# Performance work log

Measured on AMD Instinct MI355X. Metric: run time of the kernel, lower is better.

## Reference

```python
import jax, jax.numpy as jnp
import numpy as np

PH = 32          # prediction horizon (unroll steps)
HID = 512        # hidden_dim == latent_dim (output fed back as input)
OUT = 2          # output_dim
BS = 2048


def setup_inputs() -> dict:
    key = jax.random.key(0)
    ks = jax.random.split(key, 8)
    s = 1.0 / np.sqrt(HID)
    return {
        "hist": jax.random.normal(ks[0], (BS, 8, 2), dtype=jnp.float32),
        "z": jax.random.normal(ks[1], (BS, 1, HID), dtype=jnp.float32),
        # LSTMCell params (PyTorch layout: [4H, in], gate order i,f,g,o)
        "W_ih": jax.random.uniform(ks[2], (4 * HID, HID), jnp.float32, -s, s),
        "W_hh": jax.random.uniform(ks[3], (4 * HID, HID), jnp.float32, -s, s),
        "b_ih": jax.random.uniform(ks[4], (4 * HID,), jnp.float32, -s, s),
        "b_hh": jax.random.uniform(ks[5], (4 * HID,), jnp.float32, -s, s),
        # dense: hidden_dim -> output_dim
        "W_d": jax.random.uniform(ks[6], (OUT, HID), jnp.float32, -s, s),
        "b_d": jax.random.uniform(ks[7], (OUT,), jnp.float32, -s, s),
    }


def reference(hist, z, W_ih, W_hh, b_ih, b_hh, W_d, b_d):
    bs = z.shape[0]
    x0 = z.reshape(bs, -1)                       # [bs, H]
    h0 = jnp.zeros((bs, HID), dtype=z.dtype)
    c0 = jnp.zeros((bs, HID), dtype=z.dtype)

    def step(carry, _):
        x, h, c = carry
        gates = x @ W_ih.T + b_ih + h @ W_hh.T + b_hh   # [bs, 4H]
        i, f, g, o = jnp.split(gates, 4, axis=-1)
        c_new = jax.nn.sigmoid(f) * c + jax.nn.sigmoid(i) * jnp.tanh(g)
        h_new = jax.nn.sigmoid(o) * jnp.tanh(c_new)
        # output h is fed back as next input
        return (h_new, h_new, c_new), h_new

    _, hs = jax.lax.scan(step, (x0, h0, c0), None, length=PH)  # [PH, bs, H]
    out_all = jnp.swapaxes(hs, 0, 1)                           # [bs, PH, H]
    y = out_all @ W_d.T + b_d                                  # [bs, PH, OUT]
    return y
```

## Files before the change

kernel.cpp:

```cpp
#include <hip/hip_runtime.h>
#include <hip/hip_bf16.h>

#define BS_   2048
#define HID_  512
#define PH_   32

typedef _Float16 half8 __attribute__((ext_vector_type(8)));
typedef float floatx4 __attribute__((ext_vector_type(4)));

__device__ __forceinline__ float sigf(float x) { return 1.f / (1.f + __expf(-x)); }
__device__ __forceinline__ float tanhfast(float x) {
    float e = __expf(2.f * x);
    return 1.f - 2.f / (e + 1.f);
}

__global__ __launch_bounds__(256) void prep_kernel(
    const float* __restrict__ Wih, const float* __restrict__ Whh,
    const float* __restrict__ bih, const float* __restrict__ bhh,
    const float* __restrict__ z,
    _Float16* __restrict__ wih16, _Float16* __restrict__ wsum16,
    _Float16* __restrict__ z16, float* __restrict__ bsum,
    int* __restrict__ cnt)
{
    int i = blockIdx.x * 256 + threadIdx.x;
    if (i < BS_ * HID_) z16[i] = (_Float16)z[i];
    if (i < 4 * HID_ * HID_) {
        float a = Wih[i];
        wih16[i]  = (_Float16)a;
        wsum16[i] = (_Float16)(a + Whh[i]);
    }
    if (i < 4 * HID_) bsum[i] = bih[i] + bhh[i];
    if (i < 256) cnt[i] = 0;
}

__device__ __forceinline__ void stage_weights(_Float16* Wl, const _Float16* Wg,
                                              int j, int tid)
{
#pragma unroll
    for (int rep = 0; rep < 8; ++rep) {
        int idx = rep * 512 + tid;
        int n  = idx >> 6;
        int kb = idx & 63;
        int g  = n >> 4, u = n & 15;
        const half8* src = (const half8*)(Wg + ((size_t)(g * HID_ + j * 16 + u)) * HID_ + kb * 8);
        int phys = (kb & 56) | ((kb & 7) ^ (n & 7));
        *(half8*)((char*)Wl + n * 1024 + phys * 16) = *src;
    }
}

__global__ __launch_bounds__(512, 2) void lstm_persist(
    const _Float16* __restrict__ wih16, const _Float16* __restrict__ wsum16,
    const float* __restrict__ bsum, const _Float16* __restrict__ z16,
    _Float16* __restrict__ hs, int* __restrict__ cnt)
{
    __shared__ _Float16 Wl[64 * 512];

    const int tid  = threadIdx.x;
    const int ib   = blockIdx.x & 7;
    const int j    = blockIdx.x >> 3;
    const int lane = tid & 63;
    const int wv   = tid >> 6;
    const int qw   = lane >> 4;
    const int ln   = lane & 15;
    const int hid  = j * 16 + ln;

    stage_weights(Wl, wih16, j, tid);

    float bias[4];
#pragma unroll
    for (int g = 0; g < 4; ++g) bias[g] = bsum[g * HID_ + hid];

    float c[2][4];
#pragma unroll
    for (int mt = 0; mt < 2; ++mt)
#pragma unroll
        for (int r = 0; r < 4; ++r) c[mt][r] = 0.f;

    const char* Bl = (const char*)Wl;
    const int tE = (qw ^ (ln & 7)) * 16;

    __syncthreads();

    for (int t = 0; t < PH_; ++t) {
        const _Float16* xx = (t == 0) ? z16 : hs + (size_t)(t - 1) * BS_ * HID_;

        if (t >= 1) {
            if (tid == 0) {
                while (__hip_atomic_fetch_add(&cnt[ib * 32 + t - 1], 0,
                                              __ATOMIC_RELAXED,
                                              __HIP_MEMORY_SCOPE_AGENT) < 32) {
                    __builtin_amdgcn_s_sleep(1);
                }
            }
            __syncthreads();
        }

        floatx4 acc[2][4];
#pragma unroll
        for (int mt = 0; mt < 2; ++mt)
#pragma unroll
            for (int g = 0; g < 4; ++g)
                acc[mt][g] = (floatx4){bias[g], bias[g], bias[g], bias[g]};

        const _Float16* A0 = xx + (size_t)(ib * 256 + wv * 32 + ln) * HID_ + qw * 8;

        half8 a0r[4], a1r[4], bA[4], bB[4];
#pragma unroll
        for (int p = 0; p < 4; ++p) {
            a0r[p] = *(const half8*)(A0 + p * 32);
            a1r[p] = *(const half8*)(A0 + 16 * HID_ + p * 32);
        }
#pragma unroll
        for (int g = 0; g < 4; ++g)
            bA[g] = *(const half8*)(Bl + (g * 16 + ln) * 1024 + tE);

#pragma unroll
        for (int kk = 0; kk < 16; ++kk) {
            half8 ca0 = a0r[kk & 3], ca1 = a1r[kk & 3];
            if (kk < 12) {
                a0r[kk & 3] = *(const half8*)(A0 + (kk + 4) * 32);
                a1r[kk & 3] = *(const half8*)(A0 + 16 * HID_ + (kk + 4) * 32);
            }
            half8* cb = (kk & 1) ? bB : bA;
            half8* nb = (kk & 1) ? bA : bB;
            if (kk < 15) {
                int k1 = kk + 1;
#pragma unroll
                for (int g = 0; g < 4; ++g) {
                    int off = (g * 16 + ln) * 1024 + (k1 >> 1) * 128 + (tE ^ ((k1 & 1) << 6));
                    nb[g] = *(const half8*)(Bl + off);
                }
            }
#pragma unroll
            for (int g = 0; g < 4; ++g) {
                acc[0][g] = __builtin_amdgcn_mfma_f32_16x16x32_f16(ca0, cb[g], acc[0][g], 0, 0, 0);
                acc[1][g] = __builtin_amdgcn_mfma_f32_16x16x32_f16(ca1, cb[g], acc[1][g], 0, 0, 0);
            }
        }

        _Float16* hb = hs + (size_t)t * BS_ * HID_
                          + (size_t)(ib * 256 + wv * 32 + qw * 4) * HID_ + hid;
#pragma unroll
        for (int mt = 0; mt < 2; ++mt) {
#pragma unroll
            for (int r = 0; r < 4; ++r) {
                float gi = acc[mt][0][r];
                float gf = acc[mt][1][r];
                float gg = acc[mt][2][r];
                float go = acc[mt][3][r];
                float cn = sigf(gf) * c[mt][r] + sigf(gi) * tanhfast(gg);
                float hn = sigf(go) * tanhfast(cn);
                c[mt][r] = cn;
                _Float16 hf = (_Float16)hn;
                short hv;
                __builtin_memcpy(&hv, &hf, 2);
                __hip_atomic_store((short*)(hb + (size_t)(mt * 16 + r) * HID_), hv,
                                   __ATOMIC_RELAXED, __HIP_MEMORY_SCOPE_AGENT);
            }
        }

        __syncthreads();
        if (t == 0) {
            if (tid == 0)
                __hip_atomic_fetch_add(&cnt[ib * 32], 1,
                                       __ATOMIC_RELAXED, __HIP_MEMORY_SCOPE_AGENT);
            stage_weights(Wl, wsum16, j, tid);
            __syncthreads();
        } else if (t < PH_ - 1) {
            if (tid == 0)
                __hip_atomic_fetch_add(&cnt[ib * 32 + t], 1,
                                       __ATOMIC_RELAXED, __HIP_MEMORY_SCOPE_AGENT);
        }
    }
}

__global__ __launch_bounds__(256) void dense_kernel(
    const _Float16* __restrict__ hs, const float* __restrict__ Wd,
    const float* __restrict__ bd, float* __restrict__ y)
{
    int gw   = (blockIdx.x * 256 + threadIdx.x) >> 6;
    int lane = threadIdx.x & 63;
    int tt = gw & 31, b = gw >> 5;
    half8 h = *(const half8*)(hs + ((size_t)tt * BS_ + b) * HID_ + lane * 8);
    float s0 = 0.f, s1 = 0.f;
#pragma unroll
    for (int k = 0; k < 8; ++k) {
        float hv = (float)h[k];
        s0 += hv * Wd[lane * 8 + k];
        s1 += hv * Wd[HID_ + lane * 8 + k];
    }
#pragma unroll
    for (int m = 32; m >= 1; m >>= 1) {
        s0 += __shfl_xor(s0, m);
        s1 += __shfl_xor(s1, m);
    }
    if (lane == 0) {
        float* o = y + ((size_t)b * PH_ + tt) * 2;
        o[0] = s0 + bd[0];
        o[1] = s1 + bd[1];
    }
}

extern "C" void kernel_launch(void* const* d_in, const int* in_sizes, int n_in,
                              void* d_out, int out_size, void* d_ws, size_t ws_size,
                              hipStream_t stream)
{
    (void)in_sizes; (void)n_in; (void)out_size; (void)ws_size;
    const float* z   = (const float*)d_in[1];
    const float* Wih = (const float*)d_in[2];
    const float* Whh = (const float*)d_in[3];
    const float* bih = (const float*)d_in[4];
    const float* bhh = (const float*)d_in[5];
    const float* Wd  = (const float*)d_in[6];
    const float* bd  = (const float*)d_in[7];
    float* y = (float*)d_out;

    char* ws = (char*)d_ws;
    _Float16* hs     = (_Float16*)ws;
    _Float16* z16    = (_Float16*)(ws + (size_t)67108864);
    _Float16* wih16  = (_Float16*)(ws + (size_t)69206016);
    _Float16* wsum16 = (_Float16*)(ws + (size_t)71303168);
    float*    bsum   = (float*)   (ws + (size_t)73400320);
    int*      cnt    = (int*)     (ws + (size_t)73408512);

    prep_kernel<<<4096, 256, 0, stream>>>(Wih, Whh, bih, bhh, z,
                                          wih16, wsum16, z16, bsum, cnt);

    {
        const void* k = (const void*)lstm_persist;
        void* args[] = {(void*)&wih16, (void*)&wsum16, (void*)&bsum,
                        (void*)&z16, (void*)&hs, (void*)&cnt};
        hipLaunchCooperativeKernel(k, dim3(256), dim3(512), args, 0, stream);
    }

    dense_kernel<<<16384, 256, 0, stream>>>(hs, Wd, bd, y);
}
```

Before: 462.7 us.

## Split batch tile into two half-tiles with per-producer padded flags

Each persistent block now handles two 128-row half-tiles per step, one after the other. Each half-tile waits only on its own group's 32 producer flags, using one padded counter per (row group, column block) polled in parallel by a wavefront, instead of a single shared counter polled by one thread. The point is to cut atomic contention and let the second half-tile's wait overlap with other blocks' progress. In exchange there are twice as many barriers and polls per step, and the occupancy hint on the launch bounds is removed.

```diff
diff --git a/kernel.cpp b/kernel.cpp
--- a/kernel.cpp
+++ b/kernel.cpp
@@ -30,7 +30,7 @@
         wsum16[i] = (_Float16)(a + Whh[i]);
     }
     if (i < 4 * HID_) bsum[i] = bih[i] + bhh[i];
-    if (i < 256) cnt[i] = 0;
+    if (i < 8192) cnt[i] = 0;
 }
 
 __device__ __forceinline__ void stage_weights(_Float16* Wl, const _Float16* Wg,
@@ -48,7 +48,63 @@
     }
 }
 
-__global__ __launch_bounds__(512, 2) void lstm_persist(
+__device__ __forceinline__ void compute_tile(
+    const _Float16* __restrict__ xx, int ib, const char* Bl, int tE,
+    int ln, int qw, int wv, const float* bias, float* c,
+    _Float16* __restrict__ hs_t, int hid)
+{
+    floatx4 acc[4];
+#pragma unroll
+    for (int g = 0; g < 4; ++g)
+        acc[g] = (floatx4){bias[g], bias[g], bias[g], bias[g]};
+
+    const _Float16* A0 = xx + (size_t)(ib * 128 + wv * 16 + ln) * HID_ + qw * 8;
+
+    half8 ar[4], bA[4], bB[4];
+#pragma unroll
+    for (int p = 0; p < 4; ++p) ar[p] = *(const half8*)(A0 + p * 32);
+#pragma unroll
+    for (int g = 0; g < 4; ++g)
+        bA[g] = *(const half8*)(Bl + (g * 16 + ln) * 1024 + tE);
+
+#pragma unroll
+    for (int kk = 0; kk < 16; ++kk) {
+        half8 ca = ar[kk & 3];
+        if (kk < 12) ar[kk & 3] = *(const half8*)(A0 + (kk + 4) * 32);
+        half8* cb = (kk & 1) ? bB : bA;
+        half8* nb = (kk & 1) ? bA : bB;
+        if (kk < 15) {
+            int k1 = kk + 1;
+#pragma unroll
+            for (int g = 0; g < 4; ++g) {
+                int off = (g * 16 + ln) * 1024 + (k1 >> 1) * 128 + (tE ^ ((k1 & 1) << 6));
+                nb[g] = *(const half8*)(Bl + off);
+            }
+        }
+#pragma unroll
+        for (int g = 0; g < 4; ++g)
+            acc[g] = __builtin_amdgcn_mfma_f32_16x16x32_f16(ca, cb[g], acc[g], 0, 0, 0);
+    }
+
+    _Float16* hb = hs_t + (size_t)(ib * 128 + wv * 16 + qw * 4) * HID_ + hid;
+#pragma unroll
+    for (int r = 0; r < 4; ++r) {
+        float gi = acc[0][r];
+        float gf = acc[1][r];
+        float gg = acc[2][r];
+        float go = acc[3][r];
+        float cn = sigf(gf) * c[r] + sigf(gi) * tanhfast(gg);
+        float hn = sigf(go) * tanhfast(cn);
+        c[r] = cn;
+        _Float16 hf = (_Float16)hn;
+        short hv;
+        __builtin_memcpy(&hv, &hf, 2);
+        __hip_atomic_store((short*)(hb + (size_t)r * HID_), hv,
+                           __ATOMIC_RELAXED, __HIP_MEMORY_SCOPE_AGENT);
+    }
+}
+
+__global__ __launch_bounds__(512) void lstm_persist(
     const _Float16* __restrict__ wih16, const _Float16* __restrict__ wsum16,
     const float* __restrict__ bsum, const _Float16* __restrict__ z16,
     _Float16* __restrict__ hs, int* __restrict__ cnt)
@@ -56,8 +112,9 @@
     __shared__ _Float16 Wl[64 * 512];
 
     const int tid  = threadIdx.x;
-    const int ib   = blockIdx.x & 7;
-    const int j    = blockIdx.x >> 3;
+    const int j    = blockIdx.x & 31;
+    const int p    = blockIdx.x >> 5;
+    const int ibA  = 2 * p, ibB = 2 * p + 1;
     const int lane = tid & 63;
     const int wv   = tid >> 6;
     const int qw   = lane >> 4;
@@ -72,9 +129,9 @@
 
     float c[2][4];
 #pragma unroll
-    for (int mt = 0; mt < 2; ++mt)
-#pragma unroll
-        for (int r = 0; r < 4; ++r) c[mt][r] = 0.f;
+    for (int tl = 0; tl < 2; ++tl)
+#pragma unroll
+        for (int r = 0; r < 4; ++r) c[tl][r] = 0.f;
 
     const char* Bl = (const char*)Wl;
     const int tE = (qw ^ (ln & 7)) * 16;
@@ -83,93 +140,51 @@
 
     for (int t = 0; t < PH_; ++t) {
         const _Float16* xx = (t == 0) ? z16 : hs + (size_t)(t - 1) * BS_ * HID_;
+        _Float16* hs_t = hs + (size_t)t * BS_ * HID_;
 
         if (t >= 1) {
-            if (tid == 0) {
-                while (__hip_atomic_fetch_add(&cnt[ib * 32 + t - 1], 0,
-                                              __ATOMIC_RELAXED,
-                                              __HIP_MEMORY_SCOPE_AGENT) < 32) {
+            if (wv == 0) {
+                for (;;) {
+                    int v = t;
+                    if (lane < 32)
+                        v = __hip_atomic_fetch_add(&cnt[(ibA * 32 + lane) * 16], 0,
+                                                   __ATOMIC_RELAXED,
+                                                   __HIP_MEMORY_SCOPE_AGENT);
+                    if (__all(v >= t)) break;
                     __builtin_amdgcn_s_sleep(1);
                 }
             }
             __syncthreads();
         }
-
-        floatx4 acc[2][4];
-#pragma unroll
-        for (int mt = 0; mt < 2; ++mt)
-#pragma unroll
-            for (int g = 0; g < 4; ++g)
-                acc[mt][g] = (floatx4){bias[g], bias[g], bias[g], bias[g]};
-
-        const _Float16* A0 = xx + (size_t)(ib * 256 + wv * 32 + ln) * HID_ + qw * 8;
-
-        half8 a0r[4], a1r[4], bA[4], bB[4];
-#pragma unroll
-        for (int p = 0; p < 4; ++p) {
-            a0r[p] = *(const half8*)(A0 + p * 32);
-            a1r[p] = *(const half8*)(A0 + 16 * HID_ + p * 32);
-        }
-#pragma unroll
-        for (int g = 0; g < 4; ++g)
-            bA[g] = *(const half8*)(Bl + (g * 16 + ln) * 1024 + tE);
-
-#pragma unroll
-        for (int kk = 0; kk < 16; ++kk) {
-            half8 ca0 = a0r[kk & 3], ca1 = a1r[kk & 3];
-            if (kk < 12) {
-                a0r[kk & 3] = *(const half8*)(A0 + (kk + 4) * 32);
-                a1r[kk & 3] = *(const half8*)(A0 + 16 * HID_ + (kk + 4) * 32);
-            }
-            half8* cb = (kk & 1) ? bB : bA;
-            half8* nb = (kk & 1) ? bA : bB;
-            if (kk < 15) {
-                int k1 = kk + 1;
-#pragma unroll
-                for (int g = 0; g < 4; ++g) {
-                    int off = (g * 16 + ln) * 1024 + (k1 >> 1) * 128 + (tE ^ ((k1 & 1) << 6));
-                    nb[g] = *(const half8*)(Bl + off);
+        compute_tile(xx, ibA, Bl, tE, ln, qw, wv, bias, c[0], hs_t, hid);
+        __syncthreads();
+        if (tid == 0 && t < PH_ - 1)
+            __hip_atomic_fetch_add(&cnt[(ibA * 32 + j) * 16], 1,
+                                   __ATOMIC_RELAXED, __HIP_MEMORY_SCOPE_AGENT);
+
+        if (t >= 1) {
+            if (wv == 0) {
+                for (;;) {
+                    int v = t;
+                    if (lane < 32)
+                        v = __hip_atomic_fetch_add(&cnt[(ibB * 32 + lane) * 16], 0,
+                                                   __ATOMIC_RELAXED,
+                                                   __HIP_MEMORY_SCOPE_AGENT);
+                    if (__all(v >= t)) break;
+                    __builtin_amdgcn_s_sleep(1);
                 }
             }
-#pragma unroll
-            for (int g = 0; g < 4; ++g) {
-                acc[0][g] = __builtin_amdgcn_mfma_f32_16x16x32_f16(ca0, cb[g], acc[0][g], 0, 0, 0);
-                acc[1][g] = __builtin_amdgcn_mfma_f32_16x16x32_f16(ca1, cb[g], acc[1][g], 0, 0, 0);
-            }
-        }
-
-        _Float16* hb = hs + (size_t)t * BS_ * HID_
-                          + (size_t)(ib * 256 + wv * 32 + qw * 4) * HID_ + hid;
-#pragma unroll
-        for (int mt = 0; mt < 2; ++mt) {
-#pragma unroll
-            for (int r = 0; r < 4; ++r) {
-                float gi = acc[mt][0][r];
-                float gf = acc[mt][1][r];
-                float gg = acc[mt][2][r];
-                float go = acc[mt][3][r];
-                float cn = sigf(gf) * c[mt][r] + sigf(gi) * tanhfast(gg);
-                float hn = sigf(go) * tanhfast(cn);
-                c[mt][r] = cn;
-                _Float16 hf = (_Float16)hn;
-                short hv;
-                __builtin_memcpy(&hv, &hf, 2);
-                __hip_atomic_store((short*)(hb + (size_t)(mt * 16 + r) * HID_), hv,
+            __syncthreads();
+        }
+        compute_tile(xx, ibB, Bl, tE, ln, qw, wv, bias, c[1], hs_t, hid);
+        __syncthreads();
+        if (tid == 0 && t < PH_ - 1)
+            __hip_atomic_fetch_add(&cnt[(ibB * 32 + j) * 16], 1,
                                    __ATOMIC_RELAXED, __HIP_MEMORY_SCOPE_AGENT);
-            }
-        }
-
-        __syncthreads();
+
         if (t == 0) {
-            if (tid == 0)
-                __hip_atomic_fetch_add(&cnt[ib * 32], 1,
-                                       __ATOMIC_RELAXED, __HIP_MEMORY_SCOPE_AGENT);
             stage_weights(Wl, wsum16, j, tid);
             __syncthreads();
-        } else if (t < PH_ - 1) {
-            if (tid == 0)
-                __hip_atomic_fetch_add(&cnt[ib * 32 + t], 1,
-                                       __ATOMIC_RELAXED, __HIP_MEMORY_SCOPE_AGENT);
         }
     }
 }
```

Measured after the change: 478.8 us. 3.5% more time.
